# Optimization experiments

Measured on AMD Instinct MI355X. Metric: run time of the kernel, lower is better.

Reference implementation:

```python
import jax, jax.numpy as jnp
import numpy as np

# model_grid_shape (flipped ensemble grid, all equal here); E = 8 experts
GRID = (2, 2, 2)
E = GRID[0] * GRID[1] * GRID[2]
N = 524288   # query points
H = 64       # sub-model MLP hidden width


def setup_inputs() -> dict:
    key = jax.random.key(0)
    ks = jax.random.split(key, 4)
    # query coordinates in [-1, 1]^3
    x = jax.random.uniform(ks[0], (N, 3), jnp.float32, -1.0, 1.0)
    # per-expert spatial extents: axis-aligned cells tiling [-1,1]^3, in the
    # same flat order as the routing index i0 + i1*g0 + i2*g0*g1
    i = np.arange(E)
    cell = np.stack([i % GRID[0], (i // GRID[0]) % GRID[1],
                     i // (GRID[0] * GRID[1])], axis=-1).astype(np.float32)
    g = np.array(GRID, np.float32)
    extents_min = jnp.asarray(-1.0 + 2.0 * cell / g)          # [E, 3]
    extents_max = jnp.asarray(-1.0 + 2.0 * (cell + 1.0) / g)  # [E, 3]
    # per-expert SRN MLP parameters: 3 -> H -> H -> 1
    W1 = jax.random.normal(ks[1], (E, 3, H), jnp.float32) / np.sqrt(3.0)
    b1 = jnp.zeros((E, H), jnp.float32)
    W2 = jax.random.normal(ks[2], (E, H, H), jnp.float32) / np.sqrt(float(H))
    b2 = jnp.zeros((E, H), jnp.float32)
    W3 = jax.random.normal(ks[3], (E, H, 1), jnp.float32) / np.sqrt(float(H))
    b3 = jnp.zeros((E, 1), jnp.float32)
    return {"x": x, "extents_min": extents_min, "extents_max": extents_max,
            "W1": W1, "b1": b1, "W2": W2, "b2": b2, "W3": W3, "b3": b3}


def reference(x, extents_min, extents_max, W1, b1, W2, b2, W3, b3):
    # --- routing: flat expert index per point (matches torch forward) ---
    u = jnp.clip((x + 1.0) * 0.5, 0.0, 0.99)
    gvec = jnp.asarray(GRID, x.dtype)
    gi = (u * gvec).astype(jnp.int32)                       # [N, 3]
    idx = gi[:, 0] + gi[:, 1] * GRID[0] + gi[:, 2] * (GRID[0] * GRID[1])

    # --- dispatch/combine: scan over experts, masked scatter into y ---
    def body(y, args):
        i, emin, emax, w1, bb1, w2, bb2, w3, bb3 = args
        # normalize point into expert-local [-1, 1]^3
        xn = -1.0 + 2.0 * ((x - emin) / (emax - emin))      # [N, 3]
        h = jax.nn.relu(xn @ w1 + bb1)                      # [N, H]
        h = jax.nn.relu(h @ w2 + bb2)                       # [N, H]
        o = h @ w3 + bb3                                    # [N, 1]
        mask = (idx == i)[:, None]
        return jnp.where(mask, o, y), None

    y0 = jnp.zeros((x.shape[0], 1), x.dtype)
    y, _ = jax.lax.scan(
        body, y0,
        (jnp.arange(E), extents_min, extents_max, W1, b1, W2, b2, W3, b3))
    return y
```

## Files before the change

### kernel.cpp

```cpp
#include <hip/hip_runtime.h>

typedef __bf16 bf16x8 __attribute__((ext_vector_type(8)));
typedef __bf16 bf16x2 __attribute__((ext_vector_type(2)));
typedef float f32x4 __attribute__((ext_vector_type(4)));
typedef float f32x2 __attribute__((ext_vector_type(2)));

#define N_PTS 524288
#define NBLK 256
#define TPB  512
#define PPB  2048
#define CAPB 384

__device__ __forceinline__ unsigned short f2bf(float f) {
    unsigned u = __float_as_uint(f);
    u += 0x7FFFu + ((u >> 16) & 1u);
    return (unsigned short)(u >> 16);
}

__device__ __forceinline__ int route(float x0, float x1, float x2) {
    int g0 = (int)(fminf(fmaxf((x0 + 1.0f) * 0.5f, 0.0f), 0.99f) * 2.0f);
    int g1 = (int)(fminf(fmaxf((x1 + 1.0f) * 0.5f, 0.0f), 0.99f) * 2.0f);
    int g2 = (int)(fminf(fmaxf((x2 + 1.0f) * 0.5f, 0.0f), 0.99f) * 2.0f);
    return g0 + 2*g1 + 4*g2;
}

extern "C" __global__ void __launch_bounds__(512, 1) k_fused(
        const float* __restrict__ x,
        const float* __restrict__ emin, const float* __restrict__ emax,
        const float* __restrict__ W1, const float* __restrict__ b1,
        const float* __restrict__ W2, const float* __restrict__ b2,
        const float* __restrict__ W3, const float* __restrict__ b3,
        float* __restrict__ y) {
    __shared__ __align__(16) float4 pts[8][CAPB];
    __shared__ __align__(16) float4 w1s[8][64];
    __shared__ float2 eps[8][64];
    __shared__ int cnt8[8];

    int t = threadIdx.x;
    int lane = t & 63, wave = t >> 6;
    int e = wave;
    int m16 = lane & 15, g = lane >> 4, g8 = g * 8;

    if (t < 8) cnt8[t] = 0;

    const float4* x4 = (const float4*)x;
    int fb = blockIdx.x * (PPB * 3 / 4) + t * 3;
    float4 q0 = x4[fb], q1 = x4[fb + 1], q2 = x4[fb + 2];

    {
        int n = lane;
        float d0 = emax[e*3+0] - emin[e*3+0];
        float d1 = emax[e*3+1] - emin[e*3+1];
        float d2 = emax[e*3+2] - emin[e*3+2];
        float a0 = 2.0f/d0, a1 = 2.0f/d1, a2 = 2.0f/d2;
        float cc0 = -1.0f - 2.0f*emin[e*3+0]/d0;
        float cc1 = -1.0f - 2.0f*emin[e*3+1]/d1;
        float cc2 = -1.0f - 2.0f*emin[e*3+2]/d2;
        float w0 = W1[(e*3+0)*64 + n];
        float w1 = W1[(e*3+1)*64 + n];
        float w2 = W1[(e*3+2)*64 + n];
        float4 w;
        w.x = a0*w0; w.y = a1*w1; w.z = a2*w2;
        w.w = cc0*w0 + cc1*w1 + cc2*w2 + b1[e*64 + n];
        w1s[e][(n & 7) * 8 + (n >> 3)] = w;
        eps[e][n] = make_float2(b2[e*64 + n], W3[e*64 + n]);
    }
    bf16x8 A[4][2];
    #pragma unroll
    for (int mt = 0; mt < 4; ++mt) {
        #pragma unroll
        for (int half = 0; half < 2; ++half) {
            union { unsigned short us[8]; bf16x8 v; } tmp;
            #pragma unroll
            for (int j = 0; j < 8; ++j)
                tmp.us[j] = f2bf(W2[(e*64 + half*32 + g8 + j)*64 + mt*16 + m16]);
            A[mt][half] = tmp.v;
        }
    }
    float b3e = b3[e];

    float c0[4] = {q0.x, q0.w, q1.z, q2.y};
    float c1[4] = {q0.y, q1.x, q1.w, q2.z};
    float c2[4] = {q0.z, q1.y, q2.x, q2.w};
    int pbase = blockIdx.x * PPB + 4 * t;

    __syncthreads();
    #pragma unroll
    for (int i = 0; i < 4; ++i) {
        int ei = route(c0[i], c1[i], c2[i]);
        int r = atomicAdd(&cnt8[ei], 1);
        if (r < CAPB) {
            float4 v;
            v.x = c0[i]; v.y = c1[i]; v.z = c2[i];
            v.w = __uint_as_float((unsigned)(pbase + i));
            pts[ei][r] = v;
        }
    }
    __syncthreads();

    int cntw = cnt8[e]; if (cntw > CAPB) cntw = CAPB;
    for (int it0 = 0; it0 < cntw; it0 += 64) {
        float4 c[4];
        #pragma unroll
        for (int pt = 0; pt < 4; ++pt) {
            int p = it0 + pt*16 + m16;
            c[pt] = pts[e][p < cntw ? p : cntw - 1];
        }

        f32x4 acc[4][4] = {};
        #pragma unroll
        for (int half = 0; half < 2; ++half) {
            #pragma unroll
            for (int pt = 0; pt < 4; ++pt) {
                bf16x8 B;
                #pragma unroll
                for (int j = 0; j < 8; j += 2) {
                    float4 wa = w1s[e][j*8 + half*4 + g];
                    float4 wv = w1s[e][(j+1)*8 + half*4 + g];
                    float ha = fmaf(c[pt].x, wa.x, fmaf(c[pt].y, wa.y, fmaf(c[pt].z, wa.z, wa.w)));
                    float hb = fmaf(c[pt].x, wv.x, fmaf(c[pt].y, wv.y, fmaf(c[pt].z, wv.z, wv.w)));
                    f32x2 hp;
                    hp[0] = fmaxf(ha, 0.0f);
                    hp[1] = fmaxf(hb, 0.0f);
                    bf16x2 bp = __builtin_convertvector(hp, bf16x2);
                    B[j] = bp[0]; B[j+1] = bp[1];
                }
                #pragma unroll
                for (int mt = 0; mt < 4; ++mt)
                    acc[mt][pt] = __builtin_amdgcn_mfma_f32_16x16x32_bf16(A[mt][half], B, acc[mt][pt], 0, 0, 0);
            }
        }

        float s0 = 0.f, s1 = 0.f, s2 = 0.f, s3 = 0.f;
        #pragma unroll
        for (int mt = 0; mt < 4; ++mt) {
            #pragma unroll
            for (int r = 0; r < 4; ++r) {
                float2 ep = eps[e][mt*16 + g*4 + r];
                s0 = fmaf(fmaxf(acc[mt][0][r] + ep.x, 0.f), ep.y, s0);
                s1 = fmaf(fmaxf(acc[mt][1][r] + ep.x, 0.f), ep.y, s1);
                s2 = fmaf(fmaxf(acc[mt][2][r] + ep.x, 0.f), ep.y, s2);
                s3 = fmaf(fmaxf(acc[mt][3][r] + ep.x, 0.f), ep.y, s3);
            }
        }
        float sv[4] = {s0, s1, s2, s3};
        #pragma unroll
        for (int pt = 0; pt < 4; ++pt) {
            float s = sv[pt];
            s += __shfl_xor(s, 16, 64);
            s += __shfl_xor(s, 32, 64);
            if (lane < 16 && (it0 + pt*16 + m16) < cntw) {
                y[__float_as_uint(c[pt].w)] = s + b3e;
            }
        }
    }
}

extern "C" void kernel_launch(void* const* d_in, const int* in_sizes, int n_in,
                              void* d_out, int out_size, void* d_ws, size_t ws_size,
                              hipStream_t stream) {
    const float* x    = (const float*)d_in[0];
    const float* emin = (const float*)d_in[1];
    const float* emax = (const float*)d_in[2];
    const float* W1   = (const float*)d_in[3];
    const float* b1   = (const float*)d_in[4];
    const float* W2   = (const float*)d_in[5];
    const float* b2   = (const float*)d_in[6];
    const float* W3   = (const float*)d_in[7];
    const float* b3   = (const float*)d_in[8];
    float* y = (float*)d_out;
    (void)d_ws; (void)ws_size;

    k_fused<<<NBLK, TPB, 0, stream>>>(x, emin, emax, W1, b1, W2, b2, W3, b3, y);
}
```

Measured before the change: 85.61 us.

## Keep layer-1 weights in registers and vectorize epilogue with packed f32x2 math

Layer-1 folded weights are no longer staged in LDS; each lane fetches the eight features it needs via cross-lane shuffles once and keeps them in registers as packed f32x2 pairs. The layer-1 FMAs, ReLU, and the layer-2 bias/ReLU/W3 epilogue are rewritten with packed two-wide elementwise builtins, with b2 and W3 split into separate LDS arrays so pairs load as one f32x2. Launch bounds are changed to request two blocks per CU. The aim is fewer LDS reads and VALU instructions in the inner loop, at the cost of more persistent registers, which may conflict with the doubled occupancy target.

New measurement: 86.62 us. Within noise of the previous version (+1.2%).

```diff
diff --git a/kernel.cpp b/kernel.cpp
--- a/kernel.cpp
+++ b/kernel.cpp
@@ -24,7 +24,7 @@
     return g0 + 2*g1 + 4*g2;
 }
 
-extern "C" __global__ void __launch_bounds__(512, 1) k_fused(
+extern "C" __global__ void __launch_bounds__(512, 2) k_fused(
         const float* __restrict__ x,
         const float* __restrict__ emin, const float* __restrict__ emax,
         const float* __restrict__ W1, const float* __restrict__ b1,
@@ -32,8 +32,8 @@
         const float* __restrict__ W3, const float* __restrict__ b3,
         float* __restrict__ y) {
     __shared__ __align__(16) float4 pts[8][CAPB];
-    __shared__ __align__(16) float4 w1s[8][64];
-    __shared__ float2 eps[8][64];
+    __shared__ __align__(16) float b2s[8][64];
+    __shared__ __align__(16) float w3s[8][64];
     __shared__ int cnt8[8];
 
     int t = threadIdx.x;
@@ -47,6 +47,7 @@
     int fb = blockIdx.x * (PPB * 3 / 4) + t * 3;
     float4 q0 = x4[fb], q1 = x4[fb + 1], q2 = x4[fb + 2];
 
+    float4 w;
     {
         int n = lane;
         float d0 = emax[e*3+0] - emin[e*3+0];
@@ -59,12 +60,33 @@
         float w0 = W1[(e*3+0)*64 + n];
         float w1 = W1[(e*3+1)*64 + n];
         float w2 = W1[(e*3+2)*64 + n];
-        float4 w;
         w.x = a0*w0; w.y = a1*w1; w.z = a2*w2;
         w.w = cc0*w0 + cc1*w1 + cc2*w2 + b1[e*64 + n];
-        w1s[e][(n & 7) * 8 + (n >> 3)] = w;
-        eps[e][n] = make_float2(b2[e*64 + n], W3[e*64 + n]);
-    }
+        b2s[e][n] = b2[e*64 + n];
+        w3s[e][n] = W3[e*64 + n];
+    }
+
+    f32x2 wx[2][4], wy[2][4], wz[2][4], ww[2][4];
+    #pragma unroll
+    for (int h = 0; h < 2; ++h) {
+        float fx[8], fy[8], fz[8], fw[8];
+        #pragma unroll
+        for (int j = 0; j < 8; ++j) {
+            int f = h*32 + g8 + j;
+            fx[j] = __shfl(w.x, f, 64);
+            fy[j] = __shfl(w.y, f, 64);
+            fz[j] = __shfl(w.z, f, 64);
+            fw[j] = __shfl(w.w, f, 64);
+        }
+        #pragma unroll
+        for (int jp = 0; jp < 4; ++jp) {
+            wx[h][jp] = f32x2{fx[2*jp], fx[2*jp+1]};
+            wy[h][jp] = f32x2{fy[2*jp], fy[2*jp+1]};
+            wz[h][jp] = f32x2{fz[2*jp], fz[2*jp+1]};
+            ww[h][jp] = f32x2{fw[2*jp], fw[2*jp+1]};
+        }
+    }
+
     bf16x8 A[4][2];
     #pragma unroll
     for (int mt = 0; mt < 4; ++mt) {
@@ -98,6 +120,7 @@
     }
     __syncthreads();
 
+    const f32x2 zero2 = {0.f, 0.f};
     int cntw = cnt8[e]; if (cntw > CAPB) cntw = CAPB;
     for (int it0 = 0; it0 < cntw; it0 += 64) {
         float4 c[4];
@@ -109,44 +132,48 @@
 
         f32x4 acc[4][4] = {};
         #pragma unroll
-        for (int half = 0; half < 2; ++half) {
+        for (int h = 0; h < 2; ++h) {
             #pragma unroll
             for (int pt = 0; pt < 4; ++pt) {
+                f32x2 px2 = {c[pt].x, c[pt].x};
+                f32x2 py2 = {c[pt].y, c[pt].y};
+                f32x2 pz2 = {c[pt].z, c[pt].z};
                 bf16x8 B;
                 #pragma unroll
-                for (int j = 0; j < 8; j += 2) {
-                    float4 wa = w1s[e][j*8 + half*4 + g];
-                    float4 wv = w1s[e][(j+1)*8 + half*4 + g];
-                    float ha = fmaf(c[pt].x, wa.x, fmaf(c[pt].y, wa.y, fmaf(c[pt].z, wa.z, wa.w)));
-                    float hb = fmaf(c[pt].x, wv.x, fmaf(c[pt].y, wv.y, fmaf(c[pt].z, wv.z, wv.w)));
-                    f32x2 hp;
-                    hp[0] = fmaxf(ha, 0.0f);
-                    hp[1] = fmaxf(hb, 0.0f);
+                for (int jp = 0; jp < 4; ++jp) {
+                    f32x2 hp = __builtin_elementwise_fma(pz2, wz[h][jp], ww[h][jp]);
+                    hp = __builtin_elementwise_fma(py2, wy[h][jp], hp);
+                    hp = __builtin_elementwise_fma(px2, wx[h][jp], hp);
+                    hp = __builtin_elementwise_max(hp, zero2);
                     bf16x2 bp = __builtin_convertvector(hp, bf16x2);
-                    B[j] = bp[0]; B[j+1] = bp[1];
+                    B[2*jp] = bp[0]; B[2*jp+1] = bp[1];
                 }
                 #pragma unroll
                 for (int mt = 0; mt < 4; ++mt)
-                    acc[mt][pt] = __builtin_amdgcn_mfma_f32_16x16x32_bf16(A[mt][half], B, acc[mt][pt], 0, 0, 0);
+                    acc[mt][pt] = __builtin_amdgcn_mfma_f32_16x16x32_bf16(A[mt][h], B, acc[mt][pt], 0, 0, 0);
             }
         }
 
-        float s0 = 0.f, s1 = 0.f, s2 = 0.f, s3 = 0.f;
+        f32x2 s2[4] = {zero2, zero2, zero2, zero2};
         #pragma unroll
         for (int mt = 0; mt < 4; ++mt) {
             #pragma unroll
-            for (int r = 0; r < 4; ++r) {
-                float2 ep = eps[e][mt*16 + g*4 + r];
-                s0 = fmaf(fmaxf(acc[mt][0][r] + ep.x, 0.f), ep.y, s0);
-                s1 = fmaf(fmaxf(acc[mt][1][r] + ep.x, 0.f), ep.y, s1);
-                s2 = fmaf(fmaxf(acc[mt][2][r] + ep.x, 0.f), ep.y, s2);
-                s3 = fmaf(fmaxf(acc[mt][3][r] + ep.x, 0.f), ep.y, s3);
+            for (int rp = 0; rp < 2; ++rp) {
+                int f = mt*16 + g*4 + 2*rp;
+                f32x2 b2p = *(const f32x2*)&b2s[e][f];
+                f32x2 w3p = *(const f32x2*)&w3s[e][f];
+                #pragma unroll
+                for (int pt = 0; pt < 4; ++pt) {
+                    f32x2 ap = {acc[mt][pt][2*rp], acc[mt][pt][2*rp+1]};
+                    ap = ap + b2p;
+                    ap = __builtin_elementwise_max(ap, zero2);
+                    s2[pt] = __builtin_elementwise_fma(ap, w3p, s2[pt]);
+                }
             }
         }
-        float sv[4] = {s0, s1, s2, s3};
         #pragma unroll
         for (int pt = 0; pt < 4; ++pt) {
-            float s = sv[pt];
+            float s = s2[pt][0] + s2[pt][1];
             s += __shfl_xor(s, 16, 64);
             s += __shfl_xor(s, 32, 64);
             if (lane < 16 && (it0 + pt*16 + m16) < cntw) {
```
